# Kernel optimization log

Measured on AMD Instinct MI355X. Metric: run time of the kernel, lower is better.

Reference implementation:

```python
import jax, jax.numpy as jnp
import numpy as np

B, N = 4, 1024
D1, D2 = 512, 512
C = 512          # out_c = outdim_self[2] = ln_dim
H = 8            # cross_num_heads
DH = C // H      # head dim
LAYERS = 3       # cross_layer
LN_EPS = 1e-5


def _layer_norm(x, gamma, beta):
    mu = jnp.mean(x, axis=-1, keepdims=True)
    var = jnp.mean(jnp.square(x - mu), axis=-1, keepdims=True)
    return (x - mu) * jax.lax.rsqrt(var + LN_EPS) * gamma + beta


def setup_inputs() -> dict:
    key = jax.random.key(0)
    ks = jax.random.split(key, 5)
    s1, s2, sv = 1.0 / np.sqrt(D1), 1.0 / np.sqrt(D2), 1.0 / np.sqrt(D1 + D2)
    return {
        "x1": jax.random.normal(ks[0], (B, N, D1), jnp.float32),
        "x2": jax.random.normal(ks[1], (B, N, D2), jnp.float32),
        "Wq": jax.random.uniform(ks[2], (C, D1), jnp.float32, -s1, s1),
        "Wk": jax.random.uniform(ks[3], (C, D2), jnp.float32, -s2, s2),
        "Wv": jax.random.uniform(ks[4], (C, D1 + D2), jnp.float32, -sv, sv),
        "ln_gamma": jnp.ones((C,), jnp.float32),
        "ln_beta": jnp.zeros((C,), jnp.float32),
    }


def reference(x1, x2, Wq, Wk, Wv, ln_gamma, ln_beta):
    x = jnp.concatenate((x1, x2), axis=2)                      # [B,N,D1+D2]
    scale = x1.shape[-1] ** (-0.5)                             # uses x1 feature dim
    # [B,N,C] -> [B,H,N,DH]
    to_heads = lambda t: t.reshape(B, N, H, DH).transpose(0, 2, 1, 3)
    Q = to_heads(jnp.einsum('bnd,cd->bnc', x1, Wq))
    K = to_heads(jnp.einsum('bnd,cd->bnc', x2, Wk))
    V = to_heads(jnp.einsum('bnd,cd->bnc', x, Wv))

    output = None
    for _ in range(LAYERS):
        attn = jnp.einsum('bhnd,bhmd->bhnm', Q, K) * scale     # [B,H,N,N]
        mask = attn != 0
        attn = jnp.where(mask, attn, -1e20)
        attn = jax.nn.softmax(attn, axis=-1)
        attn = attn * mask
        V1 = jnp.einsum('bhnm,bhmd->bhnd', attn, V)            # [B,H,N,DH]
        V1 = V1.transpose(0, 2, 1, 3).reshape(B, N, C)
        Vr = V.transpose(0, 2, 1, 3).reshape(B, N, C)
        output = _layer_norm(V1 + Vr, ln_gamma, ln_beta)       # [B,N,C]
        V = to_heads(output)
    return output
```

## Files before the change

kernel.cpp:

```cpp
#include <hip/hip_runtime.h>


#define LOG2E 1.44269504088896f

using f32x4   = __attribute__((ext_vector_type(4))) float;
using short8  = __attribute__((ext_vector_type(8))) short;
using ushort8 = __attribute__((ext_vector_type(8))) unsigned short;
using ushort4v= __attribute__((ext_vector_type(4))) unsigned short;
using uchar8  = __attribute__((ext_vector_type(8))) unsigned char;
using uchar4v = __attribute__((ext_vector_type(4))) unsigned char;
using uchar16 = __attribute__((ext_vector_type(16))) unsigned char;

__device__ inline unsigned short f2bf(float f) {
  unsigned u = __builtin_bit_cast(unsigned, f);
  u += 0x7fffu + ((u >> 16) & 1u);
  return (unsigned short)(u >> 16);
}
__device__ inline float bf2f(unsigned short h) {
  unsigned u = (unsigned)h << 16;
  return __builtin_bit_cast(float, u);
}

__device__ inline unsigned char f2e4m3_fast(float f) {
  unsigned u = __builtin_bit_cast(unsigned, f);
  unsigned sign = (u >> 24) & 0x80u;
  unsigned a = u & 0x7fffffffu;
  unsigned v = a + (0x7ffffu + ((a >> 20) & 1u));
  unsigned m = (v >> 20) - 960u;
  m = (m > 126u) ? 126u : m;
  m = (a < 0x3c000000u) ? 0u : m;
  return (unsigned char)(sign | m);
}

__device__ inline f32x4 mfma_bf16(short8 a, short8 b, f32x4 c) {
  return __builtin_amdgcn_mfma_f32_16x16x32_bf16(a, b, c, 0, 0, 0);
}

__device__ inline void gload_lds16(const void* g, void* l) {
  __builtin_amdgcn_global_load_lds(
      (const __attribute__((address_space(1))) unsigned int*)g,
      (__attribute__((address_space(3))) unsigned int*)l, 16, 0, 0);
}

__device__ inline int swz(int row, int byte_in_row) {
  return row * 128 + (byte_in_row ^ ((row & 7) << 4));
}

__global__ __launch_bounds__(256) void k_convert_all(
    const float* __restrict__ x1, const float* __restrict__ x2,
    const float* __restrict__ Wq, const float* __restrict__ Wk,
    const float* __restrict__ Wv,
    unsigned short* __restrict__ xb, unsigned short* __restrict__ Wqb,
    unsigned short* __restrict__ Wkb, unsigned short* __restrict__ Wvb) {
  int i = blockIdx.x * 256 + threadIdx.x;
  const float* src;
  unsigned short* dst;
  if (i < 524288) {
    int e0 = i * 8, m = e0 >> 10, d = e0 & 1023;
    src = (d < 512) ? (x1 + (size_t)m * 512 + d)
                    : (x2 + (size_t)m * 512 + (d - 512));
    dst = xb + (size_t)e0;
  } else if (i < 557056) {
    int j = (i - 524288) * 8;
    src = Wq + j; dst = Wqb + j;
  } else if (i < 589824) {
    int j = (i - 557056) * 8;
    src = Wk + j; dst = Wkb + j;
  } else {
    int j = (i - 589824) * 8;
    src = Wv + j; dst = Wvb + j;
  }
  float4 a = ((const float4*)src)[0];
  float4 b = ((const float4*)src)[1];
  ushort8 o;
  o[0] = f2bf(a.x); o[1] = f2bf(a.y); o[2] = f2bf(a.z); o[3] = f2bf(a.w);
  o[4] = f2bf(b.x); o[5] = f2bf(b.y); o[6] = f2bf(b.z); o[7] = f2bf(b.w);
  *(ushort8*)dst = o;
}

__global__ __launch_bounds__(256) void k_proj(
    const unsigned short* __restrict__ xb,
    const unsigned short* __restrict__ Wqb,
    const unsigned short* __restrict__ Wkb,
    const unsigned short* __restrict__ Wvb,
    unsigned short* __restrict__ Qb, unsigned short* __restrict__ Kb,
    float* __restrict__ Vf) {
  __shared__ __align__(16) unsigned short Atile[128 * 64];
  __shared__ __align__(16) unsigned short Btile[128 * 64];

  const int id  = blockIdx.x;
  const int z   = id % 3;
  const int rem = id / 3;
  const int c0  = (rem & 3) * 128;
  const int m0  = (rem >> 2) * 128;

  const int K    = (z == 2) ? 1024 : 512;
  const int aoff = (z == 1) ? 512 : 0;
  const unsigned short* W = (z == 0) ? Wqb : (z == 1) ? Wkb : Wvb;

  const int t  = threadIdx.x;
  const int w  = t >> 6, l = t & 63;
  const int lr = l & 15, ls = l >> 4;
  const int wr = w >> 1, wc = w & 1;

  const int srow  = l >> 3;
  const int scol8 = (l & 7) * 8;

  f32x4 acc[4][4] = {};

  for (int k0 = 0; k0 < K; k0 += 64) {
#pragma unroll
    for (int j = 0; j < 4; ++j) {
      int ch  = w * 4 + j;
      int row = ch * 8 + srow;
      gload_lds16(xb + (size_t)(m0 + row) * 1024 + aoff + k0 + scol8,
                  Atile + ch * 512);
      gload_lds16(W + (size_t)(c0 + row) * K + k0 + scol8,
                  Btile + ch * 512);
    }
    __syncthreads();
#pragma unroll
    for (int ks = 0; ks < 2; ++ks) {
      short8 af[4], bf[4];
#pragma unroll
      for (int mf = 0; mf < 4; ++mf)
        af[mf] = *(const short8*)(Atile + (wr * 64 + mf * 16 + lr) * 64 +
                                  ks * 32 + ls * 8);
#pragma unroll
      for (int nf = 0; nf < 4; ++nf)
        bf[nf] = *(const short8*)(Btile + (wc * 64 + nf * 16 + lr) * 64 +
                                  ks * 32 + ls * 8);
#pragma unroll
      for (int mf = 0; mf < 4; ++mf)
#pragma unroll
        for (int nf = 0; nf < 4; ++nf)
          acc[mf][nf] = mfma_bf16(af[mf], bf[nf], acc[mf][nf]);
    }
    __syncthreads();
  }

#pragma unroll
  for (int mf = 0; mf < 4; ++mf)
#pragma unroll
    for (int nf = 0; nf < 4; ++nf)
#pragma unroll
      for (int r = 0; r < 4; ++r) {
        int m = m0 + wr * 64 + mf * 16 + ls * 4 + r;
        int c = c0 + wc * 64 + nf * 16 + lr;
        float v = acc[mf][nf][r];
        if (z == 2) {
          Vf[(size_t)m * 512 + c] = v;
        } else {
          int b = m >> 10, n = m & 1023, h = c >> 6, dh = c & 63;
          size_t idx = ((size_t)(b * 8 + h) * 1024 + n) * 64 + dh;
          (z == 0 ? Qb : Kb)[idx] = f2bf(v);
        }
      }
}

__global__ __launch_bounds__(256) void k_transpose_v(
    const float* __restrict__ Vf, void* __restrict__ Vt, int mode) {
  __shared__ unsigned short tile[64 * 66];
  const int bh = blockIdx.y;
  const int b = bh >> 3, h = bh & 7;
  const int n0 = blockIdx.x * 64;
  const int t = threadIdx.x;
  {
    int n = t >> 2, dh0 = (t & 3) * 16;
    const float* src = Vf + ((size_t)b * 1024 + n0 + n) * 512 + h * 64 + dh0;
    unsigned short* dst = tile + n * 66 + dh0;
#pragma unroll
    for (int j = 0; j < 16; j += 4) {
      float4 v = *(const float4*)(src + j);
      dst[j + 0] = f2bf(v.x); dst[j + 1] = f2bf(v.y);
      dst[j + 2] = f2bf(v.z); dst[j + 3] = f2bf(v.w);
    }
  }
  __syncthreads();
#pragma unroll
  for (int it = 0; it < 2; ++it) {
    int dh = (t >> 3) + it * 32, n8 = (t & 7) * 8;
    if (mode == 0) {
      ushort8 o;
#pragma unroll
      for (int j = 0; j < 8; ++j) o[j] = tile[(n8 + j) * 66 + dh];
      char* dst = (char*)Vt + ((size_t)(bh * 64 + dh)) * 2048 + n0 * 2 +
                  ((n8 * 2) ^ ((dh & 7) << 4));
      *(ushort8*)dst = o;
    } else {
      uchar8 o;
#pragma unroll
      for (int j = 0; j < 8; ++j)
        o[j] = f2e4m3_fast(bf2f(tile[(n8 + j) * 66 + dh]));
      int byte = n0 + n8;
      char* dst = (char*)Vt + ((size_t)(bh * 64 + dh)) * 1024 + (byte & ~127) +
                  ((byte & 127) ^ ((dh & 7) << 4));
      *(uchar8*)dst = o;
    }
  }
}

__global__ __launch_bounds__(256) void k_scores(
    const unsigned short* __restrict__ Qb,
    const unsigned short* __restrict__ Kb,
    unsigned char* __restrict__ Pmat, float* __restrict__ lsum_g) {
  __shared__ char lds[2 * 8192 + 4 * 16 * 80];
  char* kbuf0 = lds;
  char* kbuf1 = lds + 8192;
  const int id  = blockIdx.x;
  const int lid = (id & 7) * 256 + (id >> 3);
  const int bh  = lid >> 6;
  const int q0  = ((lid >> 2) & 15) * 64;
  const int kq  = lid & 3;
  const int t = threadIdx.x;
  const int w = t >> 6, l = t & 63, lr = l & 15, ls = l >> 4;
  char* pbuf = lds + 16384 + w * (16 * 80);

  const float sclog2e = 0.0637587160f;

  short8 qa[2];
  {
    const unsigned short* Qg =
        Qb + ((size_t)bh * 1024 + q0 + w * 16 + lr) * 64 + ls * 8;
    qa[0] = *(const short8*)(Qg);
    qa[1] = *(const short8*)(Qg + 32);
  }

  const unsigned short* Kg = Kb + (size_t)bh * 1024 * 64 + kq * 256 * 64;
  unsigned char* Pg = Pmat + (size_t)bh * 1024 * 1024;

  float lacc[4] = {0.f, 0.f, 0.f, 0.f};

  const int srow = t >> 3, sc8 = (t & 7) * 8;
  int4 kreg[2];
  kreg[0] = *(const int4*)(Kg + (size_t)(srow)*64 + sc8);
  kreg[1] = *(const int4*)(Kg + (size_t)(srow + 32) * 64 + sc8);
  {
    char* kb = kbuf0;
    *(int4*)(kb + swz(srow, sc8 * 2)) = kreg[0];
    *(int4*)(kb + swz(srow + 32, sc8 * 2)) = kreg[1];
  }

  for (int kc = 0; kc < 4; ++kc) {
    __syncthreads();
    char* kb  = (kc & 1) ? kbuf1 : kbuf0;
    char* kbn = (kc & 1) ? kbuf0 : kbuf1;
    if (kc < 3) {
      kreg[0] = *(const int4*)(Kg + (size_t)((kc + 1) * 64 + srow) * 64 + sc8);
      kreg[1] = *(const int4*)(Kg + (size_t)((kc + 1) * 64 + srow + 32) * 64 + sc8);
    }

    f32x4 s[4] = {};
#pragma unroll
    for (int kk = 0; kk < 2; ++kk) {
#pragma unroll
      for (int nt = 0; nt < 4; ++nt) {
        short8 bk = *(const short8*)(kb + swz(nt * 16 + lr, kk * 64 + ls * 16));
        s[nt] = mfma_bf16(qa[kk], bk, s[nt]);
      }
    }

#pragma unroll
    for (int nt = 0; nt < 4; ++nt)
#pragma unroll
      for (int r = 0; r < 4; ++r) {
        float sv = s[nt][r];
        float pv = (sv == 0.f) ? 0.f : __builtin_amdgcn_exp2f(sv * sclog2e);
        lacc[r] += pv;
        pbuf[(ls * 4 + r) * 80 + nt * 16 + lr] = (char)f2e4m3_fast(pv);
      }

    int gkc = kq * 4 + kc;
    {
      int prow = l >> 2, pchk = l & 3;
      uchar16 pv16 = *(const uchar16*)(pbuf + prow * 80 + pchk * 16);
      int n = q0 + w * 16 + prow;
      *(uchar16*)(Pg + (size_t)n * 1024 + (gkc >> 1) * 128 +
                  (((gkc & 1) * 64 + pchk * 16) ^ ((n & 7) << 4))) = pv16;
    }

    if (kc < 3) {
      *(int4*)(kbn + swz(srow, sc8 * 2)) = kreg[0];
      *(int4*)(kbn + swz(srow + 32, sc8 * 2)) = kreg[1];
    }
  }

#pragma unroll
  for (int r = 0; r < 4; ++r) {
#pragma unroll
    for (int off = 1; off < 16; off <<= 1)
      lacc[r] += __shfl_xor(lacc[r], off, 64);
  }
  if (lr == 0) {
#pragma unroll
    for (int r = 0; r < 4; ++r)
      lsum_g[kq * 32768 + (size_t)bh * 1024 + q0 + w * 16 + ls * 4 + r] =
          lacc[r];
  }
}

__global__ __launch_bounds__(256) void k_pv(
    const unsigned char* __restrict__ Pmat,
    const unsigned char* __restrict__ Vt,
    const float* __restrict__ lsum_g, float* __restrict__ V1a,
    float* __restrict__ V1b) {
  __shared__ __align__(16) char Ab[2][8192];
  __shared__ __align__(16) char Bb[2][8192];
  const int id  = blockIdx.x;
  const int lid = (id & 7) * 128 + (id >> 3);
  const int head = lid >> 5;
  const int n0   = ((lid >> 1) & 15) * 64;
  const int mh   = lid & 1;
  const int t = threadIdx.x;
  const int w = t >> 6, l = t & 63, lr = l & 15, ls = l >> 4;

  const char* Pg = (const char*)(Pmat + (size_t)head * 1024 * 1024) +
                   (size_t)n0 * 1024 + mh * 512;
  const char* Vg = (const char*)(Vt + (size_t)head * 64 * 1024) + mh * 512;

  const int srow = w * 16 + (l >> 3);
  const int sc16 = (l & 7) * 16;

  f32x4 acc[4] = {};

  auto STAGE = [&](int buf, int kc) {
#pragma unroll
    for (int j = 0; j < 2; ++j) {
      int row = srow + j * 8;
      gload_lds16(Pg + (size_t)row * 1024 + kc * 128 + sc16,
                  &Ab[buf][w * 2048 + j * 1024]);
      gload_lds16(Vg + (size_t)row * 1024 + kc * 128 + sc16,
                  &Bb[buf][w * 2048 + j * 1024]);
    }
  };

  STAGE(0, 0);
  __syncthreads();
  int cur = 0;
  for (int kc = 0; kc < 4; ++kc) {
    if (kc < 3) STAGE(cur ^ 1, kc + 1);
#pragma unroll
    for (int ks = 0; ks < 4; ++ks) {
      long af = *(const long*)(&Ab[cur][swz(w * 16 + lr, ks * 32 + ls * 8)]);
#pragma unroll
      for (int nf = 0; nf < 4; ++nf) {
        long bf8 = *(const long*)(&Bb[cur][swz(nf * 16 + lr, ks * 32 + ls * 8)]);
        acc[nf] = __builtin_amdgcn_mfma_f32_16x16x32_fp8_fp8(af, bf8, acc[nf],
                                                             0, 0, 0);
      }
    }
    __syncthreads();
    cur ^= 1;
  }

  float* V1 = mh ? V1b : V1a;
  const int b = head >> 3, h = head & 7;
#pragma unroll
  for (int r = 0; r < 4; ++r) {
    int n = n0 + w * 16 + ls * 4 + r;
    size_t li = (size_t)head * 1024 + n;
    float lv = lsum_g[li] + lsum_g[32768 + li] + lsum_g[65536 + li] +
               lsum_g[98304 + li];
    float rinv = (lv > 0.f) ? 1.f / lv : 0.f;
#pragma unroll
    for (int nf = 0; nf < 4; ++nf)
      V1[((size_t)b * 1024 + n) * 512 + h * 64 + nf * 16 + lr] =
          acc[nf][r] * rinv;
  }
}

__global__ __launch_bounds__(256) void k_ln_t(
    const float* __restrict__ V1a, const float* __restrict__ V1b,
    const float* __restrict__ Vf_in,
    const float* __restrict__ gamma, const float* __restrict__ beta,
    float* __restrict__ Vf_out, void* __restrict__ Vt, int mode) {
  __shared__ unsigned short tile[4 * 520];
  const int blk = blockIdx.x;
  const int b  = blk >> 8;
  const int n0 = (blk & 255) * 4;
  const int t = threadIdx.x;
  const int row = t >> 6;
  const int l = t & 63;
  const int c0 = l * 8;
  const size_t base = ((size_t)b * 1024 + n0 + row) * 512 + c0;

  float x[8];
  float s = 0.f, sq = 0.f;
#pragma unroll
  for (int j = 0; j < 8; j += 4) {
    float4 a0 = *(const float4*)(V1a + base + j);
    float4 a1 = *(const float4*)(V1b + base + j);
    float4 v = *(const float4*)(Vf_in + base + j);
    float4 y = {a0.x + a1.x + v.x, a0.y + a1.y + v.y, a0.z + a1.z + v.z,
                a0.w + a1.w + v.w};
    x[j + 0] = y.x; x[j + 1] = y.y; x[j + 2] = y.z; x[j + 3] = y.w;
    s  += y.x + y.y + y.z + y.w;
    sq += y.x * y.x + y.y * y.y + y.z * y.z + y.w * y.w;
  }
#pragma unroll
  for (int off = 1; off < 64; off <<= 1) {
    s  += __shfl_xor(s, off, 64);
    sq += __shfl_xor(sq, off, 64);
  }
  float mu   = s * (1.f / 512.f);
  float var  = sq * (1.f / 512.f) - mu * mu;
  float rstd = rsqrtf(var + 1e-5f);

  unsigned short* trow = tile + row * 520 + c0;
#pragma unroll
  for (int j = 0; j < 8; j += 4) {
    float4 g = *(const float4*)(gamma + c0 + j);
    float4 bb = *(const float4*)(beta + c0 + j);
    float4 y;
    y.x = (x[j + 0] - mu) * rstd * g.x + bb.x;
    y.y = (x[j + 1] - mu) * rstd * g.y + bb.y;
    y.z = (x[j + 2] - mu) * rstd * g.z + bb.z;
    y.w = (x[j + 3] - mu) * rstd * g.w + bb.w;
    *(float4*)(Vf_out + base + j) = y;
    if (mode != 2) {
      trow[j + 0] = f2bf(y.x); trow[j + 1] = f2bf(y.y);
      trow[j + 2] = f2bf(y.z); trow[j + 3] = f2bf(y.w);
    }
  }
  if (mode == 2) return;
  __syncthreads();

#pragma unroll
  for (int it = 0; it < 2; ++it) {
    int d = t + it * 256;
    int h = d >> 6, dh = d & 63;
    int sw = (dh & 7) << 4;
    if (mode == 0) {
      ushort4v o;
#pragma unroll
      for (int j = 0; j < 4; ++j) o[j] = tile[j * 520 + d];
      int byte0 = n0 * 2;
      char* dst = (char*)Vt + ((size_t)((b * 8 + h) * 64 + dh)) * 2048 +
                  (byte0 & ~127) + ((byte0 & 127) ^ sw);
      *(ushort4v*)dst = o;
    } else {
      uchar4v o;
#pragma unroll
      for (int j = 0; j < 4; ++j) o[j] = f2e4m3_fast(bf2f(tile[j * 520 + d]));
      char* dst = (char*)Vt + ((size_t)((b * 8 + h) * 64 + dh)) * 1024 +
                  (n0 & ~127) + ((n0 & 127) ^ sw);
      *(uchar4v*)dst = o;
    }
  }
}

__global__ __launch_bounds__(256) void k_attn(
    const unsigned short* __restrict__ Qb,
    const unsigned short* __restrict__ Kb,
    const unsigned short* __restrict__ Vt,
    float* __restrict__ V1) {
  __shared__ char lds[8192 + 8192 + 4 * 16 * 144];
  char* kbuf = lds;
  char* vbuf = lds + 8192;
  const int bh = blockIdx.y;
  const int q0 = blockIdx.x * 64;
  const int t = threadIdx.x;
  const int w = t >> 6, l = t & 63, lr = l & 15, ls = l >> 4;
  char* pbuf = lds + 16384 + w * (16 * 144);

  const float scale = 0.044194173824159216f;

  short8 qa[2];
  {
    const unsigned short* Qg =
        Qb + ((size_t)bh * 1024 + q0 + w * 16 + lr) * 64 + ls * 8;
    qa[0] = *(const short8*)(Qg);
    qa[1] = *(const short8*)(Qg + 32);
  }

  f32x4 O[4] = {};
  float mrow[4], lrow[4];
#pragma unroll
  for (int r = 0; r < 4; ++r) { mrow[r] = -INFINITY; lrow[r] = 0.f; }

  const unsigned short* Kg = Kb + (size_t)bh * 1024 * 64;
  const char* Vg = (const char*)(Vt + (size_t)bh * 64 * 1024);

  for (int kc = 0; kc < 16; ++kc) {
    {
      int row = t >> 3;
      int c8  = (t & 7) * 8;
#pragma unroll
      for (int it = 0; it < 2; ++it) {
        int rr = row + it * 32;
        int4 kv = *(const int4*)(Kg + (size_t)(kc * 64 + rr) * 64 + c8);
        *(int4*)(kbuf + swz(rr, c8 * 2)) = kv;
        int swv = (rr & 7) << 4;
        int4 vv = *(const int4*)(Vg + (size_t)rr * 2048 + kc * 128 +
                                 ((c8 * 2) ^ swv));
        *(int4*)(vbuf + swz(rr, c8 * 2)) = vv;
      }
    }
    __syncthreads();

    f32x4 s[4] = {};
#pragma unroll
    for (int kk = 0; kk < 2; ++kk) {
#pragma unroll
      for (int nt = 0; nt < 4; ++nt) {
        short8 bk = *(const short8*)(kbuf + swz(nt * 16 + lr, kk * 64 + ls * 16));
        s[nt] = mfma_bf16(qa[kk], bk, s[nt]);
      }
    }

    float p[4][4];
    float cmax[4];
#pragma unroll
    for (int r = 0; r < 4; ++r) cmax[r] = -INFINITY;
#pragma unroll
    for (int nt = 0; nt < 4; ++nt)
#pragma unroll
      for (int r = 0; r < 4; ++r) {
        float sv = s[nt][r];
        p[nt][r] = (sv == 0.f) ? -INFINITY : sv * scale;
        cmax[r] = fmaxf(cmax[r], p[nt][r]);
      }
#pragma unroll
    for (int r = 0; r < 4; ++r)
#pragma unroll
      for (int off = 1; off < 16; off <<= 1)
        cmax[r] = fmaxf(cmax[r], __shfl_xor(cmax[r], off, 64));

    float alpha[4];
#pragma unroll
    for (int r = 0; r < 4; ++r) {
      float mnew = fmaxf(mrow[r], cmax[r]);
      alpha[r] = (mnew == -INFINITY) ? 1.f : exp2f((mrow[r] - mnew) * LOG2E);
      mrow[r] = mnew;
    }
    float lsum[4] = {0.f, 0.f, 0.f, 0.f};
#pragma unroll
    for (int nt = 0; nt < 4; ++nt)
#pragma unroll
      for (int r = 0; r < 4; ++r) {
        float pv = (p[nt][r] == -INFINITY)
                       ? 0.f
                       : exp2f((p[nt][r] - mrow[r]) * LOG2E);
        p[nt][r] = pv;
        lsum[r] += pv;
      }
#pragma unroll
    for (int r = 0; r < 4; ++r) {
#pragma unroll
      for (int off = 1; off < 16; off <<= 1)
        lsum[r] += __shfl_xor(lsum[r], off, 64);
      lrow[r] = lrow[r] * alpha[r] + lsum[r];
    }
#pragma unroll
    for (int dt = 0; dt < 4; ++dt)
#pragma unroll
      for (int r = 0; r < 4; ++r) O[dt][r] *= alpha[r];

#pragma unroll
    for (int nt = 0; nt < 4; ++nt)
#pragma unroll
      for (int r = 0; r < 4; ++r)
        *(unsigned short*)(pbuf + (ls * 4 + r) * 144 + (nt * 16 + lr) * 2) =
            f2bf(p[nt][r]);

#pragma unroll
    for (int kk = 0; kk < 2; ++kk) {
      short8 pa = *(const short8*)(pbuf + lr * 144 + kk * 64 + ls * 16);
#pragma unroll
      for (int dt = 0; dt < 4; ++dt) {
        short8 bv = *(const short8*)(vbuf + swz(dt * 16 + lr, kk * 64 + ls * 16));
        O[dt] = mfma_bf16(pa, bv, O[dt]);
      }
    }
    __syncthreads();
  }

  float rinv[4];
#pragma unroll
  for (int r = 0; r < 4; ++r) rinv[r] = (lrow[r] > 0.f) ? 1.f / lrow[r] : 0.f;
  const int b = bh >> 3, h = bh & 7;
#pragma unroll
  for (int dt = 0; dt < 4; ++dt)
#pragma unroll
    for (int r = 0; r < 4; ++r) {
      int n = q0 + w * 16 + ls * 4 + r;
      int c = h * 64 + dt * 16 + lr;
      V1[((size_t)b * 1024 + n) * 512 + c] = O[dt][r] * rinv[r];
    }
}

extern "C" void kernel_launch(void* const* d_in, const int* in_sizes, int n_in,
                              void* d_out, int out_size, void* d_ws,
                              size_t ws_size, hipStream_t stream) {
  const float* x1    = (const float*)d_in[0];
  const float* x2    = (const float*)d_in[1];
  const float* Wq    = (const float*)d_in[2];
  const float* Wk    = (const float*)d_in[3];
  const float* Wv    = (const float*)d_in[4];
  const float* gamma = (const float*)d_in[5];
  const float* beta  = (const float*)d_in[6];
  float* out = (float*)d_out;
  char* ws = (char*)d_ws;

  const size_t MB = 1u << 20;
  unsigned short* xb  = (unsigned short*)(ws);
  unsigned short* Wqb = (unsigned short*)(ws + 8 * MB);
  unsigned short* Wkb = (unsigned short*)(ws + 8 * MB + 512 * 1024);
  unsigned short* Wvb = (unsigned short*)(ws + 9 * MB);
  unsigned short* Qb  = (unsigned short*)(ws + 10 * MB);
  unsigned short* Kb  = (unsigned short*)(ws + 14 * MB);
  void*           Vt  = (void*)(ws + 18 * MB);
  float*          Vf  = (float*)(ws + 22 * MB);
  float*          V1a = (float*)(ws + 30 * MB);
  float*          lsm = (float*)(ws + 38 * MB);
  unsigned char*  Pm  = (unsigned char*)(ws + 39 * MB);
  float*          V1b = (float*)(ws);

  const bool bigws = ws_size >= (size_t)71 * MB;

  k_convert_all<<<2560, 256, 0, stream>>>(x1, x2, Wq, Wk, Wv, xb, Wqb, Wkb,
                                          Wvb);
  k_proj<<<384, 256, 0, stream>>>(xb, Wqb, Wkb, Wvb, Qb, Kb, Vf);

  if (bigws) {
    k_transpose_v<<<dim3(16, 32), 256, 0, stream>>>(Vf, Vt, 1);
    k_scores<<<2048, 256, 0, stream>>>(Qb, Kb, Pm, lsm);
    for (int layer = 0; layer < 3; ++layer) {
      k_pv<<<1024, 256, 0, stream>>>(Pm, (const unsigned char*)Vt, lsm, V1a,
                                     V1b);
      if (layer < 2)
        k_ln_t<<<1024, 256, 0, stream>>>(V1a, V1b, Vf, gamma, beta, Vf, Vt, 1);
      else
        k_ln_t<<<1024, 256, 0, stream>>>(V1a, V1b, Vf, gamma, beta, out, Vt, 2);
    }
  } else {
    hipMemsetAsync(V1b, 0, 8 * MB, stream);
    k_transpose_v<<<dim3(16, 32), 256, 0, stream>>>(Vf, Vt, 0);
    for (int layer = 0; layer < 3; ++layer) {
      k_attn<<<dim3(16, 32), 256, 0, stream>>>(Qb, Kb,
                                               (const unsigned short*)Vt, V1a);
      if (layer < 2)
        k_ln_t<<<1024, 256, 0, stream>>>(V1a, V1b, Vf, gamma, beta, Vf, Vt, 0);
      else
        k_ln_t<<<1024, 256, 0, stream>>>(V1a, V1b, Vf, gamma, beta, out, Vt, 2);
    }
  }
}
```

Baseline: 125.8 us.

## Fuse V fp8 transpose into projection epilogue and store V1 partials as bf16

The V projection epilogue now also writes the swizzled fp8 transposed V directly, so the separate transpose kernel launch is dropped on the big-workspace path. The attention/PV kernels store their V1 partial outputs as bf16 instead of fp32, halving the traffic that the layernorm kernel reads. The cost is lower precision in the residual partials and scattered 4-byte stores in the projection epilogue.

```diff
diff --git a/kernel.cpp b/kernel.cpp
--- a/kernel.cpp
+++ b/kernel.cpp
@@ -84,7 +84,7 @@
     const unsigned short* __restrict__ Wkb,
     const unsigned short* __restrict__ Wvb,
     unsigned short* __restrict__ Qb, unsigned short* __restrict__ Kb,
-    float* __restrict__ Vf) {
+    float* __restrict__ Vf, unsigned char* __restrict__ VtF8, int writeVt) {
   __shared__ __align__(16) unsigned short Atile[128 * 64];
   __shared__ __align__(16) unsigned short Btile[128 * 64];
 
@@ -142,24 +142,37 @@
 #pragma unroll
   for (int mf = 0; mf < 4; ++mf)
 #pragma unroll
-    for (int nf = 0; nf < 4; ++nf)
-#pragma unroll
-      for (int r = 0; r < 4; ++r) {
-        int m = m0 + wr * 64 + mf * 16 + ls * 4 + r;
-        int c = c0 + wc * 64 + nf * 16 + lr;
-        float v = acc[mf][nf][r];
-        if (z == 2) {
-          Vf[(size_t)m * 512 + c] = v;
-        } else {
+    for (int nf = 0; nf < 4; ++nf) {
+      int m = m0 + wr * 64 + mf * 16 + ls * 4;
+      int c = c0 + wc * 64 + nf * 16 + lr;
+      if (z == 2) {
+#pragma unroll
+        for (int r = 0; r < 4; ++r)
+          Vf[(size_t)(m + r) * 512 + c] = acc[mf][nf][r];
+        if (writeVt) {
           int b = m >> 10, n = m & 1023, h = c >> 6, dh = c & 63;
+          uchar4v o;
+#pragma unroll
+          for (int r = 0; r < 4; ++r) o[r] = f2e4m3_fast(acc[mf][nf][r]);
+          char* dst = (char*)VtF8 +
+                      ((size_t)((b * 8 + h) * 64 + dh)) * 1024 + (n & ~127) +
+                      ((n & 127) ^ ((dh & 7) << 4));
+          *(uchar4v*)dst = o;
+        }
+      } else {
+#pragma unroll
+        for (int r = 0; r < 4; ++r) {
+          int mm = m + r;
+          int b = mm >> 10, n = mm & 1023, h = c >> 6, dh = c & 63;
           size_t idx = ((size_t)(b * 8 + h) * 1024 + n) * 64 + dh;
-          (z == 0 ? Qb : Kb)[idx] = f2bf(v);
+          (z == 0 ? Qb : Kb)[idx] = f2bf(acc[mf][nf][r]);
         }
       }
+    }
 }
 
 __global__ __launch_bounds__(256) void k_transpose_v(
-    const float* __restrict__ Vf, void* __restrict__ Vt, int mode) {
+    const float* __restrict__ Vf, void* __restrict__ Vt) {
   __shared__ unsigned short tile[64 * 66];
   const int bh = blockIdx.y;
   const int b = bh >> 3, h = bh & 7;
@@ -180,23 +193,12 @@
 #pragma unroll
   for (int it = 0; it < 2; ++it) {
     int dh = (t >> 3) + it * 32, n8 = (t & 7) * 8;
-    if (mode == 0) {
-      ushort8 o;
-#pragma unroll
-      for (int j = 0; j < 8; ++j) o[j] = tile[(n8 + j) * 66 + dh];
-      char* dst = (char*)Vt + ((size_t)(bh * 64 + dh)) * 2048 + n0 * 2 +
-                  ((n8 * 2) ^ ((dh & 7) << 4));
-      *(ushort8*)dst = o;
-    } else {
-      uchar8 o;
-#pragma unroll
-      for (int j = 0; j < 8; ++j)
-        o[j] = f2e4m3_fast(bf2f(tile[(n8 + j) * 66 + dh]));
-      int byte = n0 + n8;
-      char* dst = (char*)Vt + ((size_t)(bh * 64 + dh)) * 1024 + (byte & ~127) +
-                  ((byte & 127) ^ ((dh & 7) << 4));
-      *(uchar8*)dst = o;
-    }
+    ushort8 o;
+#pragma unroll
+    for (int j = 0; j < 8; ++j) o[j] = tile[(n8 + j) * 66 + dh];
+    char* dst = (char*)Vt + ((size_t)(bh * 64 + dh)) * 2048 + n0 * 2 +
+                ((n8 * 2) ^ ((dh & 7) << 4));
+    *(ushort8*)dst = o;
   }
 }
 
@@ -302,8 +304,8 @@
 __global__ __launch_bounds__(256) void k_pv(
     const unsigned char* __restrict__ Pmat,
     const unsigned char* __restrict__ Vt,
-    const float* __restrict__ lsum_g, float* __restrict__ V1a,
-    float* __restrict__ V1b) {
+    const float* __restrict__ lsum_g, unsigned short* __restrict__ V1a,
+    unsigned short* __restrict__ V1b) {
   __shared__ __align__(16) char Ab[2][8192];
   __shared__ __align__(16) char Bb[2][8192];
   const int id  = blockIdx.x;
@@ -353,7 +355,7 @@
     cur ^= 1;
   }
 
-  float* V1 = mh ? V1b : V1a;
+  unsigned short* V1 = mh ? V1b : V1a;
   const int b = head >> 3, h = head & 7;
 #pragma unroll
   for (int r = 0; r < 4; ++r) {
@@ -365,12 +367,13 @@
 #pragma unroll
     for (int nf = 0; nf < 4; ++nf)
       V1[((size_t)b * 1024 + n) * 512 + h * 64 + nf * 16 + lr] =
-          acc[nf][r] * rinv;
+          f2bf(acc[nf][r] * rinv);
   }
 }
 
 __global__ __launch_bounds__(256) void k_ln_t(
-    const float* __restrict__ V1a, const float* __restrict__ V1b,
+    const unsigned short* __restrict__ V1a,
+    const unsigned short* __restrict__ V1b,
     const float* __restrict__ Vf_in,
     const float* __restrict__ gamma, const float* __restrict__ beta,
     float* __restrict__ Vf_out, void* __restrict__ Vt, int mode) {
@@ -386,16 +389,19 @@
 
   float x[8];
   float s = 0.f, sq = 0.f;
-#pragma unroll
-  for (int j = 0; j < 8; j += 4) {
-    float4 a0 = *(const float4*)(V1a + base + j);
-    float4 a1 = *(const float4*)(V1b + base + j);
-    float4 v = *(const float4*)(Vf_in + base + j);
-    float4 y = {a0.x + a1.x + v.x, a0.y + a1.y + v.y, a0.z + a1.z + v.z,
-                a0.w + a1.w + v.w};
-    x[j + 0] = y.x; x[j + 1] = y.y; x[j + 2] = y.z; x[j + 3] = y.w;
-    s  += y.x + y.y + y.z + y.w;
-    sq += y.x * y.x + y.y * y.y + y.z * y.z + y.w * y.w;
+  {
+    ushort8 a0 = *(const ushort8*)(V1a + base);
+    ushort8 a1 = *(const ushort8*)(V1b + base);
+    float4 v0 = *(const float4*)(Vf_in + base);
+    float4 v1 = *(const float4*)(Vf_in + base + 4);
+#pragma unroll
+    for (int j = 0; j < 8; ++j) {
+      float vf = (j < 4) ? ((const float*)&v0)[j] : ((const float*)&v1)[j - 4];
+      float y = bf2f(a0[j]) + bf2f(a1[j]) + vf;
+      x[j] = y;
+      s += y;
+      sq += y * y;
+    }
   }
 #pragma unroll
   for (int off = 1; off < 64; off <<= 1) {
@@ -453,7 +459,7 @@
     const unsigned short* __restrict__ Qb,
     const unsigned short* __restrict__ Kb,
     const unsigned short* __restrict__ Vt,
-    float* __restrict__ V1) {
+    unsigned short* __restrict__ V1) {
   __shared__ char lds[8192 + 8192 + 4 * 16 * 144];
   char* kbuf = lds;
   char* vbuf = lds + 8192;
@@ -585,7 +591,7 @@
     for (int r = 0; r < 4; ++r) {
       int n = q0 + w * 16 + ls * 4 + r;
       int c = h * 64 + dt * 16 + lr;
-      V1[((size_t)b * 1024 + n) * 512 + c] = O[dt][r] * rinv[r];
+      V1[((size_t)b * 1024 + n) * 512 + c] = f2bf(O[dt][r] * rinv[r]);
     }
 }
 
@@ -611,19 +617,19 @@
   unsigned short* Kb  = (unsigned short*)(ws + 14 * MB);
   void*           Vt  = (void*)(ws + 18 * MB);
   float*          Vf  = (float*)(ws + 22 * MB);
-  float*          V1a = (float*)(ws + 30 * MB);
+  unsigned short* V1a = (unsigned short*)(ws + 30 * MB);
   float*          lsm = (float*)(ws + 38 * MB);
   unsigned char*  Pm  = (unsigned char*)(ws + 39 * MB);
-  float*          V1b = (float*)(ws);
+  unsigned short* V1b = (unsigned short*)(ws);
 
   const bool bigws = ws_size >= (size_t)71 * MB;
 
   k_convert_all<<<2560, 256, 0, stream>>>(x1, x2, Wq, Wk, Wv, xb, Wqb, Wkb,
                                           Wvb);
-  k_proj<<<384, 256, 0, stream>>>(xb, Wqb, Wkb, Wvb, Qb, Kb, Vf);
+  k_proj<<<384, 256, 0, stream>>>(xb, Wqb, Wkb, Wvb, Qb, Kb, Vf,
+                                  (unsigned char*)Vt, bigws ? 1 : 0);
 
   if (bigws) {
-    k_transpose_v<<<dim3(16, 32), 256, 0, stream>>>(Vf, Vt, 1);
     k_scores<<<2048, 256, 0, stream>>>(Qb, Kb, Pm, lsm);
     for (int layer = 0; layer < 3; ++layer) {
       k_pv<<<1024, 256, 0, stream>>>(Pm, (const unsigned char*)Vt, lsm, V1a,
@@ -634,8 +640,8 @@
         k_ln_t<<<1024, 256, 0, stream>>>(V1a, V1b, Vf, gamma, beta, out, Vt, 2);
     }
   } else {
-    hipMemsetAsync(V1b, 0, 8 * MB, stream);
-    k_transpose_v<<<dim3(16, 32), 256, 0, stream>>>(Vf, Vt, 0);
+    hipMemsetAsync(V1b, 0, 4 * MB, stream);
+    k_transpose_v<<<dim3(16, 32), 256, 0, stream>>>(Vf, Vt);
     for (int layer = 0; layer < 3; ++layer) {
       k_attn<<<dim3(16, 32), 256, 0, stream>>>(Qb, Kb,
                                                (const unsigned short*)Vt, V1a);
```

Result: faster. 118.4 us (-5.9%).
